# Kernel optimization log

Hardware: AMD Instinct MI355X
Metric: run time of the kernel (lower is better)

## Reference

```python
import jax, jax.numpy as jnp
import numpy as np

DIM = 3072
HEADS = 24
HD = 128
FF = 4 * DIM
EPS = 1e-6
SCALE_SHIFT = 1.0


def _ln(x):
    # LayerNorm, elementwise_affine=False
    mu = jnp.mean(x, axis=-1, keepdims=True)
    var = jnp.mean(jnp.square(x - mu), axis=-1, keepdims=True)
    return (x - mu) * jax.lax.rsqrt(var + EPS)


def _rms(x, w):
    # RMSNorm over head_dim with learned weight
    ms = jnp.mean(jnp.square(x), axis=-1, keepdims=True)
    return x * jax.lax.rsqrt(ms + EPS) * w


def _rope(x, cos, sin):
    # x: [B,S,H,D], cos/sin: [S,D]; interleaved rotate-half (diffusers style)
    xr = x.reshape(*x.shape[:-1], -1, 2)
    x1, x2 = xr[..., 0], xr[..., 1]
    rot = jnp.stack([-x2, x1], axis=-1).reshape(x.shape)
    return x * cos[None, :, None, :] + rot * sin[None, :, None, :]


def _mod_params(temb, w, b):
    m = jax.nn.silu(temb) @ w + b  # [B, 6*DIM]
    B = m.shape[0]
    m = m.reshape(B, -1, 6).transpose(0, 2, 1).reshape(B, -1)  # reorder to 6 blocks of DIM
    return jnp.split(m, 2, axis=-1)  # mod1, mod2 each [B, 3*DIM]


def _modulate(x, mp):
    shift, scale, gate = jnp.split(mp, 3, axis=-1)
    scale = scale + SCALE_SHIFT
    return x * scale[:, None, :] + shift[:, None, :], gate[:, None, :]


def setup_inputs() -> dict:
    key = jax.random.key(0)
    ks = jax.random.split(key, 32)
    B, ST, SI = 1, 512, 1024
    S = ST + SI
    r = lambda k, shp, s=1.0: jax.random.normal(k, shp, dtype=jnp.float32) * s
    W = 0.02  # weight init scale
    ang = jax.random.uniform(ks[5], (S, HD), minval=0.0, maxval=2 * np.pi)
    inp = {
        "hidden_states": r(ks[0], (B, SI, DIM)),
        "encoder_hidden_states": r(ks[1], (B, ST, DIM)),
        "encoder_hidden_states_mask": jnp.ones((B, ST), jnp.float32),
        "temb": r(ks[2], (B, DIM)),
        "rope_cos": jnp.cos(ang),
        "rope_sin": jnp.sin(ang),
        "w_img_mod": r(ks[6], (DIM, 6 * DIM), W), "b_img_mod": r(ks[7], (6 * DIM,), W),
        "w_txt_mod": r(ks[8], (DIM, 6 * DIM), W), "b_txt_mod": r(ks[9], (6 * DIM,), W),
        "norm_q_w": jnp.ones((HD,), jnp.float32), "norm_k_w": jnp.ones((HD,), jnp.float32),
        "norm_added_q_w": jnp.ones((HD,), jnp.float32), "norm_added_k_w": jnp.ones((HD,), jnp.float32),
        "w_qkv": r(ks[10], (DIM, 3 * DIM), W), "b_qkv": r(ks[11], (3 * DIM,), W),
        "w_add_qkv": r(ks[12], (DIM, 3 * DIM), W), "b_add_qkv": r(ks[13], (3 * DIM,), W),
        "w_out": r(ks[14], (DIM, DIM), W), "b_out": r(ks[15], (DIM,), W),
        "w_add_out": r(ks[16], (DIM, DIM), W), "b_add_out": r(ks[17], (DIM,), W),
        "w_img_mlp1": r(ks[18], (DIM, FF), W), "b_img_mlp1": r(ks[19], (FF,), W),
        "w_img_mlp2": r(ks[20], (FF, DIM), W), "b_img_mlp2": r(ks[21], (DIM,), W),
        "w_txt_mlp1": r(ks[22], (DIM, FF), W), "b_txt_mlp1": r(ks[23], (FF,), W),
        "w_txt_mlp2": r(ks[24], (FF, DIM), W), "b_txt_mlp2": r(ks[25], (DIM,), W),
    }
    return inp


def reference(hidden_states, encoder_hidden_states, encoder_hidden_states_mask, temb,
              rope_cos, rope_sin,
              w_img_mod, b_img_mod, w_txt_mod, b_txt_mod,
              norm_q_w, norm_k_w, norm_added_q_w, norm_added_k_w,
              w_qkv, b_qkv, w_add_qkv, b_add_qkv,
              w_out, b_out, w_add_out, b_add_out,
              w_img_mlp1, b_img_mlp1, w_img_mlp2, b_img_mlp2,
              w_txt_mlp1, b_txt_mlp1, w_txt_mlp2, b_txt_mlp2):
    B, SI, _ = hidden_states.shape
    ST = encoder_hidden_states.shape[1]

    img_mod1, img_mod2 = _mod_params(temb, w_img_mod, b_img_mod)
    txt_mod1, txt_mod2 = _mod_params(temb, w_txt_mod, b_txt_mod)

    img_m, img_g1 = _modulate(_ln(hidden_states), img_mod1)
    txt_m, txt_g1 = _modulate(_ln(encoder_hidden_states), txt_mod1)

    # joint attention
    iq, ik, iv = jnp.split(img_m @ w_qkv + b_qkv, 3, axis=-1)
    tq, tk, tv = jnp.split(txt_m @ w_add_qkv + b_add_qkv, 3, axis=-1)
    iq = _rms(iq.reshape(B, SI, HEADS, HD), norm_q_w)
    ik = _rms(ik.reshape(B, SI, HEADS, HD), norm_k_w)
    iv = iv.reshape(B, SI, HEADS, HD)
    tq = _rms(tq.reshape(B, ST, HEADS, HD), norm_added_q_w)
    tk = _rms(tk.reshape(B, ST, HEADS, HD), norm_added_k_w)
    tv = tv.reshape(B, ST, HEADS, HD)
    q = jnp.concatenate([tq, iq], axis=1)  # [B,S,H,D], txt first
    k = jnp.concatenate([tk, ik], axis=1)
    v = jnp.concatenate([tv, iv], axis=1)
    q = _rope(q, rope_cos, rope_sin)
    k = _rope(k, rope_cos, rope_sin)
    scores = jnp.einsum('bqhd,bkhd->bhqk', q, k) / np.float32(np.sqrt(HD))
    probs = jax.nn.softmax(scores, axis=-1)
    attn = jnp.einsum('bhqk,bkhd->bqhd', probs, v).reshape(B, ST + SI, HEADS * HD)

    txt_a = attn[:, :ST] @ w_add_out + b_add_out
    img_a = attn[:, ST:] @ w_out + b_out
    hidden = hidden_states + img_g1 * img_a
    enc = encoder_hidden_states + txt_g1 * txt_a

    # fused GELU(tanh) MLPs with modulation
    img_m2, img_g2 = _modulate(_ln(hidden), img_mod2)
    img_mlp = jax.nn.gelu(img_m2 @ w_img_mlp1 + b_img_mlp1, approximate=True) @ w_img_mlp2 + b_img_mlp2
    hidden = hidden + img_g2 * img_mlp

    txt_m2, txt_g2 = _modulate(_ln(enc), txt_mod2)
    txt_mlp = jax.nn.gelu(txt_m2 @ w_txt_mlp1 + b_txt_mlp1, approximate=True) @ w_txt_mlp2 + b_txt_mlp2
    enc = enc + txt_g2 * txt_mlp

    return enc, hidden
```

## Files before the change

### kernel.cpp

```cpp
#include <hip/hip_runtime.h>

#define DIMX 3072
#define STX 512
#define SIX 1024
#define SQX 1536
#define FFX 12288

typedef __attribute__((ext_vector_type(4))) float f32x4;
typedef __attribute__((ext_vector_type(8))) __bf16 bf16x8;
typedef __attribute__((ext_vector_type(4))) int i32x4;
typedef __attribute__((ext_vector_type(4))) unsigned short u16x4;

__device__ __forceinline__ unsigned short f2bf(float f){
  unsigned u = __builtin_bit_cast(unsigned, f);
  u += 0x7FFFu + ((u>>16)&1u);
  return (unsigned short)(u>>16);
}
__device__ __forceinline__ unsigned short usbf(float x){
  return __builtin_bit_cast(unsigned short, (__bf16)x);
}
__device__ __forceinline__ float bf2f(unsigned short h){
  unsigned u = ((unsigned)h)<<16;
  return __builtin_bit_cast(float, u);
}
__device__ __forceinline__ float gelu_tanh(float x){
  float x3 = x*x*x;
  float z = 0.7978845608028654f*(x + 0.044715f*x3);
  z = fminf(fmaxf(z, -15.f), 15.f);
  float e = exp2f(z*2.8853900817779268f);
  float th = (e-1.f)/(e+1.f);
  return 0.5f*x*(1.f+th);
}

__device__ __forceinline__ void gload16(const void* g, void* l){
  __builtin_amdgcn_global_load_lds(
      (const __attribute__((address_space(1))) void*)g,
      (__attribute__((address_space(3))) void*)l,
      16, 0, 0);
}


__global__ void k_silu(const float* __restrict__ temb, float* __restrict__ out){
  int i = blockIdx.x*256 + threadIdx.x;
  if(i < DIMX){
    float x = temb[i];
    out[i] = x / (1.f + exp2f(-x*1.4426950408889634f));
  }
}

__global__ void k_modinit(const float* __restrict__ b_img, const float* __restrict__ b_txt,
                          float* __restrict__ mod){
  int idx = blockIdx.x*256 + threadIdx.x;
  int mat = idx / 18432; int r = idx % 18432;
  int i = r/6, j = r%6;
  const float* b = mat ? b_txt : b_img;
  mod[mat*18432 + j*3072 + i] = b[r];
}

__global__ void k_modgemv(const float* __restrict__ w_img, const float* __restrict__ w_txt,
                          const float* __restrict__ silu_t, float* __restrict__ mod){
  int bz = blockIdx.x;
  int ks = bz & 7; bz >>= 3;
  int nc = bz % 18; int mat = bz / 18;
  const float* W = mat ? w_txt : w_img;
  __shared__ float st[384];
  int k0 = ks*384;
  for(int i = threadIdx.x; i < 384; i += 256) st[i] = silu_t[k0+i];
  __syncthreads();
  int n0 = nc*1024 + threadIdx.x*4;
  float ax=0.f, ay=0.f, az=0.f, aw=0.f;
  const float* Wp = W + (size_t)k0*18432 + n0;
  #pragma unroll 4
  for(int k=0;k<384;k++){
    float4 w = *(const float4*)(Wp + (size_t)k*18432);
    float s = st[k];
    ax += s*w.x; ay += s*w.y; az += s*w.z; aw += s*w.w;
  }
  float* md = mod + mat*18432;
  float vals[4] = {ax, ay, az, aw};
  #pragma unroll
  for(int j=0;j<4;j++){
    int n = n0+j; int i = n/6, jj = n%6;
    atomicAdd(&md[jj*3072 + i], vals[j]);
  }
}

__global__ void k_initC(float* __restrict__ out, const float* __restrict__ res,
                        const float* __restrict__ gate, const float* __restrict__ bias){
  int i = (blockIdx.x*256 + threadIdx.x)*4;
  int col = i % 3072;
  float4 r = *(const float4*)(res + i);
  float4 g = *(const float4*)(gate + col);
  float4 b = *(const float4*)(bias + col);
  float4 o = {r.x + g.x*b.x, r.y + g.y*b.y, r.z + g.z*b.z, r.w + g.w*b.w};
  *(float4*)(out + i) = o;
}

__global__ void k_lnmod(const float* __restrict__ x, const float* __restrict__ modp,
                        unsigned short* __restrict__ out){
  int row = blockIdx.x, t = threadIdx.x;
  const float* xr = x + (size_t)row*DIMX;
  float4 v0 = *(const float4*)(xr + t*4);
  float4 v1 = *(const float4*)(xr + 1024 + t*4);
  float4 v2 = *(const float4*)(xr + 2048 + t*4);
  float s  = v0.x+v0.y+v0.z+v0.w + v1.x+v1.y+v1.z+v1.w + v2.x+v2.y+v2.z+v2.w;
  float s2 = v0.x*v0.x+v0.y*v0.y+v0.z*v0.z+v0.w*v0.w
           + v1.x*v1.x+v1.y*v1.y+v1.z*v1.z+v1.w*v1.w
           + v2.x*v2.x+v2.y*v2.y+v2.z*v2.z+v2.w*v2.w;
  #pragma unroll
  for(int o=32;o>0;o>>=1){ s += __shfl_xor(s,o); s2 += __shfl_xor(s2,o); }
  __shared__ float rs_[4], rs2_[4];
  int wid = t>>6;
  if((t&63)==0){ rs_[wid]=s; rs2_[wid]=s2; }
  __syncthreads();
  float S  = rs_[0]+rs_[1]+rs_[2]+rs_[3];
  float S2 = rs2_[0]+rs2_[1]+rs2_[2]+rs2_[3];
  float mu = S*(1.f/3072.f);
  float var = S2*(1.f/3072.f) - mu*mu;
  float rstd = rsqrtf(var + 1e-6f);
  #pragma unroll
  for(int j=0;j<3;j++){
    int c = j*1024 + t*4;
    float4 sh = *(const float4*)(modp + c);
    float4 sc = *(const float4*)(modp + 3072 + c);
    float4 xv = (j==0)?v0:((j==1)?v1:v2);
    unsigned short h0 = f2bf((xv.x-mu)*rstd*(sc.x+1.f)+sh.x);
    unsigned short h1 = f2bf((xv.y-mu)*rstd*(sc.y+1.f)+sh.y);
    unsigned short h2 = f2bf((xv.z-mu)*rstd*(sc.z+1.f)+sh.z);
    unsigned short h3 = f2bf((xv.w-mu)*rstd*(sc.w+1.f)+sh.w);
    unsigned long long pk = (unsigned long long)(h0 | ((unsigned)h1<<16))
                          | ((unsigned long long)(h2 | ((unsigned)h3<<16))<<32);
    *(unsigned long long*)(out + (size_t)row*DIMX + c) = pk;
  }
}

__global__ void k_rmsrope(const unsigned short* __restrict__ qkv_txt,
                          const unsigned short* __restrict__ qkv_img,
                          const float* __restrict__ nqw, const float* __restrict__ nkw,
                          const float* __restrict__ naqw, const float* __restrict__ nakw,
                          const float* __restrict__ cosb, const float* __restrict__ sinb,
                          unsigned short* __restrict__ Q, unsigned short* __restrict__ K,
                          unsigned short* __restrict__ V){
  int s = blockIdx.x, h = blockIdx.y, t = threadIdx.x;
  bool txt = s < STX;
  const unsigned short* src = txt ? (qkv_txt + (size_t)s*9216)
                                  : (qkv_img + (size_t)(s-STX)*9216);
  const float* qw = txt ? naqw : nqw;
  const float* kw = txt ? nakw : nkw;
  int d0 = 2*t;
  float q1 = bf2f(src[h*128 + d0]),        q2 = bf2f(src[h*128 + d0 + 1]);
  float k1 = bf2f(src[3072 + h*128 + d0]), k2 = bf2f(src[3072 + h*128 + d0 + 1]);
  float v1 = bf2f(src[6144 + h*128 + d0]), v2 = bf2f(src[6144 + h*128 + d0 + 1]);
  float sq = q1*q1 + q2*q2, sk = k1*k1 + k2*k2;
  #pragma unroll
  for(int o=32;o>0;o>>=1){ sq += __shfl_xor(sq,o); sk += __shfl_xor(sk,o); }
  float rq = rsqrtf(sq*(1.f/128.f) + 1e-6f);
  float rk = rsqrtf(sk*(1.f/128.f) + 1e-6f);
  q1 *= rq*qw[d0]; q2 *= rq*qw[d0+1];
  k1 *= rk*kw[d0]; k2 *= rk*kw[d0+1];
  float c1 = cosb[(size_t)s*128 + d0], c2 = cosb[(size_t)s*128 + d0 + 1];
  float s1 = sinb[(size_t)s*128 + d0], s2 = sinb[(size_t)s*128 + d0 + 1];
  float Q1 = q1*c1 - q2*s1, Q2 = q2*c2 + q1*s2;
  float K1 = k1*c1 - k2*s1, K2 = k2*c2 + k1*s2;
  size_t o = ((size_t)s*24 + h)*128 + d0;
  Q[o] = f2bf(Q1); Q[o+1] = f2bf(Q2);
  K[o] = f2bf(K1); K[o+1] = f2bf(K2);
  V[o] = f2bf(v1); V[o+1] = f2bf(v2);
}

__global__ void k_vtrans(const unsigned short* __restrict__ V, unsigned short* __restrict__ VT){
  __shared__ unsigned short tile[64][136];
  int st = blockIdx.x, h = blockIdx.y, t = threadIdx.x;
  int s0 = st*64;
  {
    int s = t>>2;
    #pragma unroll
    for(int i=0;i<4;i++){
      int oct = ((t&3)<<2) + i;
      i32x4 d = *(const i32x4*)(V + ((size_t)(s0+s)*24 + h)*128 + oct*8);
      *(i32x4*)&tile[s][oct*8] = d;
    }
  }
  __syncthreads();
  {
    int d0 = t>>3; int strip = t&7;
    #pragma unroll
    for(int i=0;i<4;i++){
      int d = d0 + i*32;
      unsigned short h8[8];
      #pragma unroll
      for(int j=0;j<8;j++) h8[j] = tile[strip*8 + j][d];
      unsigned a0 = h8[0] | ((unsigned)h8[1]<<16);
      unsigned a1 = h8[2] | ((unsigned)h8[3]<<16);
      unsigned a2 = h8[4] | ((unsigned)h8[5]<<16);
      unsigned a3 = h8[6] | ((unsigned)h8[7]<<16);
      i32x4 dv = {(int)a0,(int)a1,(int)a2,(int)a3};
      *(i32x4*)(VT + ((size_t)h*128 + d)*1536 + s0 + strip*8) = dv;
    }
  }
}

__global__ __launch_bounds__(256,2) void k_fattn(
    const unsigned short* __restrict__ Q,
    const unsigned short* __restrict__ Kb,
    const unsigned short* __restrict__ VT,
    unsigned short* __restrict__ O)
{
  __shared__ unsigned short Kls[4][64][32];
  __shared__ unsigned short Vls[2][128][32];
  __shared__ unsigned short Pls[128][72];
  const int t = threadIdx.x;
  const int qb = blockIdx.x, h = blockIdx.y;
  const int lane = t&63, w = t>>6;
  const int lr = lane&15, lk = lane>>4;
  const float SC  = 0.08838834764831845f;
  const float L2E = 1.4426950408889634f;

  bf16x8 qf[2][4];
  {
    const unsigned short* qp = Q + ((size_t)(qb*128 + w*32 + lr)*3072) + h*128 + lk*8;
    #pragma unroll
    for(int mf=0;mf<2;mf++)
      #pragma unroll
      for(int ks=0;ks<4;ks++)
        qf[mf][ks] = *(const bf16x8*)(qp + (size_t)mf*16*3072 + ks*32);
  }

  f32x4 o[2][8];
  #pragma unroll
  for(int i=0;i<2;i++)
    #pragma unroll
    for(int j=0;j<8;j++) o[i][j] = (f32x4){0.f,0.f,0.f,0.f};
  float mrow[2][4], lrow[2][4];
  #pragma unroll
  for(int i=0;i<2;i++)
    #pragma unroll
    for(int r=0;r<4;r++){ mrow[i][r] = -3.0e30f; lrow[i][r] = 0.f; }

  for(int kv0=0; kv0<SQX; kv0+=64){
    __syncthreads();
    {
      const unsigned short* kp = Kb + ((size_t)(kv0 + (lane>>2))*3072) + h*128 + w*32 + (lane&3)*8;
      #pragma unroll
      for(int i=0;i<4;i++)
        gload16(kp + (size_t)i*16*3072, &Kls[w][i*16][0]);
    }
    {
      int c = w>>1;
      const unsigned short* vp = VT + ((size_t)(h*128 + (w&1)*64 + (lane>>2)))*1536 + kv0 + c*32 + (lane&3)*8;
      #pragma unroll
      for(int j=0;j<4;j++)
        gload16(vp + (size_t)j*16*1536, &Vls[c][(w&1)*64 + j*16][0]);
    }
    __syncthreads();

    f32x4 s[2][4];
    #pragma unroll
    for(int mf=0;mf<2;mf++)
      #pragma unroll
      for(int nf=0;nf<4;nf++) s[mf][nf] = (f32x4){0.f,0.f,0.f,0.f};
    #pragma unroll
    for(int ks=0;ks<4;ks++){
      bf16x8 kf[4];
      #pragma unroll
      for(int nf=0;nf<4;nf++) kf[nf] = *(const bf16x8*)&Kls[ks][nf*16+lr][lk*8];
      #pragma unroll
      for(int mf=0;mf<2;mf++)
        #pragma unroll
        for(int nf=0;nf<4;nf++)
          s[mf][nf] = __builtin_amdgcn_mfma_f32_16x16x32_bf16(qf[mf][ks], kf[nf], s[mf][nf], 0,0,0);
    }

    #pragma unroll
    for(int mf=0;mf<2;mf++){
      #pragma unroll
      for(int r=0;r<4;r++){
        float v = fmaxf(fmaxf(s[mf][0][r], s[mf][1][r]), fmaxf(s[mf][2][r], s[mf][3][r]));
        #pragma unroll
        for(int d=1; d<16; d<<=1) v = fmaxf(v, __shfl_xor(v, d));
        float nm = fmaxf(mrow[mf][r], v*SC);
        float fac = exp2f((mrow[mf][r]-nm)*L2E);
        mrow[mf][r] = nm;
        float rs = 0.f;
        #pragma unroll
        for(int nf=0;nf<4;nf++){
          float p = exp2f((s[mf][nf][r]*SC - nm)*L2E);
          s[mf][nf][r] = p;
          rs += p;
        }
        #pragma unroll
        for(int d=1; d<16; d<<=1) rs += __shfl_xor(rs, d);
        lrow[mf][r] = lrow[mf][r]*fac + rs;
        #pragma unroll
        for(int nf=0;nf<8;nf++) o[mf][nf][r] *= fac;
      }
    }

    #pragma unroll
    for(int mf=0;mf<2;mf++)
      #pragma unroll
      for(int nf=0;nf<4;nf++)
        #pragma unroll
        for(int r=0;r<4;r++)
          Pls[w*32 + mf*16 + lk*4 + r][nf*16 + lr] = usbf(s[mf][nf][r]);

    #pragma unroll
    for(int ks2=0; ks2<2; ks2++){
      bf16x8 pa[2];
      #pragma unroll
      for(int mf=0;mf<2;mf++)
        pa[mf] = *(const bf16x8*)&Pls[w*32 + mf*16 + lr][ks2*32 + lk*8];
      #pragma unroll
      for(int nf=0;nf<8;nf++){
        bf16x8 vf = *(const bf16x8*)&Vls[ks2][nf*16+lr][lk*8];
        #pragma unroll
        for(int mf=0;mf<2;mf++)
          o[mf][nf] = __builtin_amdgcn_mfma_f32_16x16x32_bf16(pa[mf], vf, o[mf][nf], 0,0,0);
      }
    }
  }

  #pragma unroll
  for(int mf=0;mf<2;mf++){
    float inv[4];
    #pragma unroll
    for(int r=0;r<4;r++) inv[r] = 1.f/lrow[mf][r];
    #pragma unroll
    for(int nf=0;nf<8;nf++){
      #pragma unroll
      for(int r=0;r<4;r++){
        size_t row = (size_t)qb*128 + w*32 + mf*16 + lk*4 + r;
        size_t col = (size_t)h*128 + nf*16 + lr;
        O[row*3072 + col] = usbf(o[mf][nf][r]*inv[r]);
      }
    }
  }
}

__global__ __launch_bounds__(256,4) void k_gemmW(
    const unsigned short* __restrict__ A, long lda,
    const float* __restrict__ W, long ldw,
    const float* __restrict__ bias,
    void* __restrict__ Cp, long ldc,
    int K, int KS, int mode,
    const float* __restrict__ gate)
{
  __shared__ unsigned short Als[128*32];
  __shared__ float Wls[32*128];
  __shared__ unsigned short Bls[128*40];
  const int t = threadIdx.x;
  const int bn = blockIdx.x, bm = blockIdx.y;
  const int zs = blockIdx.z;
  const int Kc = K / KS, kbeg = zs*Kc, kend = kbeg + Kc;

  const unsigned short* Ab = A + (size_t)bm*128*lda;
  const float* Wb = W + (size_t)bn*128;

  const int lane = t & 63, wid = t>>6, wr = wid>>1, wc = wid&1;
  const int lr = lane & 15, lk = lane>>4;
  const int srow = (lane>>2);
  const int soff = (lane&3)*8;
  const int wrow = (lane>>5);
  const int wcol = (lane&31)*4;
  const int ck = (t&7)*4;
  const int cn = (t>>3)*4;

  f32x4 acc[4][4];
  #pragma unroll
  for(int i=0;i<4;i++)
    #pragma unroll
    for(int j=0;j<4;j++) acc[i][j] = {0.f,0.f,0.f,0.f};

  for(int k0=kbeg; k0<kend; k0+=32){
    __syncthreads();
    gload16(Ab + (size_t)(     wid*16 + srow)*lda + k0 + soff, Als + (     wid*16)*32);
    gload16(Ab + (size_t)(64 + wid*16 + srow)*lda + k0 + soff, Als + (64 + wid*16)*32);
    #pragma unroll
    for(int i=0;i<4;i++){
      int r0 = wid*8 + i*2;
      gload16(Wb + (size_t)(k0 + r0 + wrow)*ldw + wcol, Wls + r0*128);
    }
    __syncthreads();
    {
      f32x4 r0 = *(const f32x4*)&Wls[(ck+0)*128 + cn];
      f32x4 r1 = *(const f32x4*)&Wls[(ck+1)*128 + cn];
      f32x4 r2 = *(const f32x4*)&Wls[(ck+2)*128 + cn];
      f32x4 r3 = *(const f32x4*)&Wls[(ck+3)*128 + cn];
      #pragma unroll
      for(int jn=0;jn<4;jn++){
        u16x4 pk = { usbf(r0[jn]), usbf(r1[jn]), usbf(r2[jn]), usbf(r3[jn]) };
        *(u16x4*)&Bls[(cn+jn)*40 + ck] = pk;
      }
    }
    __syncthreads();
    bf16x8 af[4], bfr[4];
    #pragma unroll
    for(int mf=0;mf<4;mf++) af[mf]  = *(const bf16x8*)&Als[(wr*64 + mf*16 + lr)*32 + lk*8];
    #pragma unroll
    for(int nf=0;nf<4;nf++) bfr[nf] = *(const bf16x8*)&Bls[(wc*64 + nf*16 + lr)*40 + lk*8];
    #pragma unroll
    for(int mf=0;mf<4;mf++)
      #pragma unroll
      for(int nf=0;nf<4;nf++)
        acc[mf][nf] = __builtin_amdgcn_mfma_f32_16x16x32_bf16(af[mf], bfr[nf], acc[mf][nf], 0,0,0);
  }

  unsigned short* C16 = (unsigned short*)Cp;
  float* C32 = (float*)Cp;
  #pragma unroll
  for(int mf=0;mf<4;mf++){
    #pragma unroll
    for(int nf=0;nf<4;nf++){
      #pragma unroll
      for(int r=0;r<4;r++){
        size_t row = (size_t)bm*128 + wr*64 + mf*16 + lk*4 + r;
        size_t col = (size_t)bn*128 + wc*64 + nf*16 + lr;
        float v = acc[mf][nf][r];
        if(mode==0){
          C16[row*ldc + col] = f2bf(v + (bias ? bias[col] : 0.f));
        } else if(mode==1){
          C16[row*ldc + col] = f2bf(gelu_tanh(v + (bias ? bias[col] : 0.f)));
        } else {
          float g = gate ? gate[col] : 1.f;
          atomicAdd(&C32[row*ldc + col], g*v);
        }
      }
    }
  }
}


extern "C" void kernel_launch(void* const* d_in, const int* in_sizes, int n_in,
                              void* d_out, int out_size, void* d_ws, size_t ws_size,
                              hipStream_t stream){
  const float* hidden_states = (const float*)d_in[0];
  const float* enc_states    = (const float*)d_in[1];
  const float* temb          = (const float*)d_in[3];
  const float* rope_cos      = (const float*)d_in[4];
  const float* rope_sin      = (const float*)d_in[5];
  const float* w_img_mod     = (const float*)d_in[6];
  const float* b_img_mod     = (const float*)d_in[7];
  const float* w_txt_mod     = (const float*)d_in[8];
  const float* b_txt_mod     = (const float*)d_in[9];
  const float* norm_q_w      = (const float*)d_in[10];
  const float* norm_k_w      = (const float*)d_in[11];
  const float* norm_aq_w     = (const float*)d_in[12];
  const float* norm_ak_w     = (const float*)d_in[13];
  const float* w_qkv   = (const float*)d_in[14];
  const float* b_qkv   = (const float*)d_in[15];
  const float* w_aqkv  = (const float*)d_in[16];
  const float* b_aqkv  = (const float*)d_in[17];
  const float* w_out_  = (const float*)d_in[18];
  const float* b_out_  = (const float*)d_in[19];
  const float* w_aout  = (const float*)d_in[20];
  const float* b_aout  = (const float*)d_in[21];
  const float* w_mlp1i = (const float*)d_in[22];
  const float* b_mlp1i = (const float*)d_in[23];
  const float* w_mlp2i = (const float*)d_in[24];
  const float* b_mlp2i = (const float*)d_in[25];
  const float* w_mlp1t = (const float*)d_in[26];
  const float* b_mlp1t = (const float*)d_in[27];
  const float* w_mlp2t = (const float*)d_in[28];
  const float* b_mlp2t = (const float*)d_in[29];

  char* ws = (char*)d_ws;
  float* mod    = (float*)(ws + 0);
  float* silu_t = (float*)(ws + 147456);
  unsigned short* imgm = (unsigned short*)(ws + 159744);
  unsigned short* txtm = (unsigned short*)(ws + 6451200);
  float* hid = (float*)(ws + 9596928);
  float* enc = (float*)(ws + 22179840);
  unsigned short* Qb  = (unsigned short*)(ws + 47345664);
  unsigned short* Kb  = (unsigned short*)(ws + 56782848);
  unsigned short* Vb  = (unsigned short*)(ws + 66220032);
  unsigned short* attnb = (unsigned short*)(ws + 66220032);
  unsigned short* VTb = (unsigned short*)(ws + 75657216);
  unsigned short* qkvi = (unsigned short*)(ws + 141717504);
  unsigned short* qkvt = (unsigned short*)(ws + 160591872);
  unsigned short* mlph = (unsigned short*)(ws + 103968768);

  float* out_enc = (float*)d_out;
  float* out_hid = (float*)d_out + (size_t)STX*DIMX;

  k_silu<<<12,256,0,stream>>>(temb, silu_t);
  k_modinit<<<144,256,0,stream>>>(b_img_mod, b_txt_mod, mod);
  k_modgemv<<<288,256,0,stream>>>(w_img_mod, w_txt_mod, silu_t, mod);

  k_lnmod<<<SIX,256,0,stream>>>(hidden_states, mod + 0,     imgm);
  k_lnmod<<<STX,256,0,stream>>>(enc_states,    mod + 18432, txtm);

  k_gemmW<<<dim3(72,8,1),256,0,stream>>>(imgm,3072, w_qkv,9216, b_qkv,
      qkvi,9216, 3072,1, 0, nullptr);
  k_gemmW<<<dim3(72,4,1),256,0,stream>>>(txtm,3072, w_aqkv,9216, b_aqkv,
      qkvt,9216, 3072,1, 0, nullptr);

  k_rmsrope<<<dim3(1536,24),64,0,stream>>>(qkvt, qkvi, norm_q_w, norm_k_w,
      norm_aq_w, norm_ak_w, rope_cos, rope_sin, Qb, Kb, Vb);
  k_vtrans<<<dim3(24,24),256,0,stream>>>(Vb, VTb);

  k_fattn<<<dim3(12,24),256,0,stream>>>(Qb, Kb, VTb, attnb);

  k_initC<<<512*3,256,0,stream>>>(enc, enc_states, mod + 18432 + 2*3072, b_aout);
  k_initC<<<1024*3,256,0,stream>>>(hid, hidden_states, mod + 2*3072, b_out_);
  k_gemmW<<<dim3(24,4,8),256,0,stream>>>(attnb,3072, w_aout,3072, nullptr,
      enc,3072, 3072,8, 3, mod + 18432 + 2*3072);
  k_gemmW<<<dim3(24,8,4),256,0,stream>>>(attnb + (size_t)512*3072,3072, w_out_,3072, nullptr,
      hid,3072, 3072,4, 3, mod + 2*3072);

  k_lnmod<<<SIX,256,0,stream>>>(hid, mod + 3*3072, imgm);
  k_gemmW<<<dim3(96,8,1),256,0,stream>>>(imgm,3072, w_mlp1i,12288, b_mlp1i,
      mlph,12288, 3072,1, 1, nullptr);
  k_initC<<<1024*3,256,0,stream>>>(out_hid, hid, mod + 5*3072, b_mlp2i);
  k_gemmW<<<dim3(24,8,4),256,0,stream>>>(mlph,12288, w_mlp2i,3072, nullptr,
      out_hid,3072, 12288,4, 3, mod + 5*3072);

  k_lnmod<<<STX,256,0,stream>>>(enc, mod + 18432 + 3*3072, txtm);
  k_gemmW<<<dim3(96,4,1),256,0,stream>>>(txtm,3072, w_mlp1t,12288, b_mlp1t,
      mlph,12288, 3072,1, 1, nullptr);
  k_initC<<<512*3,256,0,stream>>>(out_enc, enc, mod + 18432 + 5*3072, b_mlp2t);
  k_gemmW<<<dim3(24,4,8),256,0,stream>>>(mlph,12288, w_mlp2t,3072, nullptr,
      out_enc,3072, 12288,8, 3, mod + 18432 + 5*3072);
}
```

Before: 1.251 ms.

## Double-buffer k_gemmW shared tiles and convert fp32 weights in registers

Rewrites the k_gemmW main loop to double-buffer the A and bf16 B tiles in LDS. The next K-slice is prefetched while MFMAs run on the current one, and the loop drops from three barriers per step to one. Weights are now loaded straight into registers as float4, converted to bf16 and stored transposed into LDS, so the fp32 weight staging buffer goes away. The cost is more register pressure from the prefetched weights and a second set of LDS buffers, which could lower occupancy under launch_bounds(256,4).

After: 1.195 ms. 1.05x faster.

```diff
diff --git a/kernel.cpp b/kernel.cpp
--- a/kernel.cpp
+++ b/kernel.cpp
@@ -345,9 +345,8 @@
     int K, int KS, int mode,
     const float* __restrict__ gate)
 {
-  __shared__ unsigned short Als[128*32];
-  __shared__ float Wls[32*128];
-  __shared__ unsigned short Bls[128*40];
+  __shared__ unsigned short Als[2][128*32];
+  __shared__ unsigned short Bls[2][128*40];
   const int t = threadIdx.x;
   const int bn = blockIdx.x, bm = blockIdx.y;
   const int zs = blockIdx.z;
@@ -360,10 +359,8 @@
   const int lr = lane & 15, lk = lane>>4;
   const int srow = (lane>>2);
   const int soff = (lane&3)*8;
-  const int wrow = (lane>>5);
-  const int wcol = (lane&31)*4;
-  const int ck = (t&7)*4;
-  const int cn = (t>>3)*4;
+  const int wcb = (t&31)*4;
+  const int wrb = (t>>5)*4;
 
   f32x4 acc[4][4];
   #pragma unroll
@@ -371,38 +368,56 @@
     #pragma unroll
     for(int j=0;j<4;j++) acc[i][j] = {0.f,0.f,0.f,0.f};
 
+  float4 wreg[4];
+
+  gload16(Ab + (size_t)(     wid*16 + srow)*lda + kbeg + soff, &Als[0][(     wid*16)*32]);
+  gload16(Ab + (size_t)(64 + wid*16 + srow)*lda + kbeg + soff, &Als[0][(64 + wid*16)*32]);
+  #pragma unroll
+  for(int j=0;j<4;j++)
+    wreg[j] = *(const float4*)(Wb + (size_t)(kbeg + wrb + j)*ldw + wcb);
+  #pragma unroll
+  for(int i=0;i<4;i++){
+    u16x4 pk = { usbf(wreg[0][i]), usbf(wreg[1][i]), usbf(wreg[2][i]), usbf(wreg[3][i]) };
+    *(u16x4*)&Bls[0][(wcb+i)*40 + wrb] = pk;
+  }
+  __syncthreads();
+
+  unsigned short* AlsC = &Als[0][0]; unsigned short* AlsN = &Als[1][0];
+  unsigned short* BlsC = &Bls[0][0]; unsigned short* BlsN = &Bls[1][0];
+
   for(int k0=kbeg; k0<kend; k0+=32){
+    const bool has = (k0 + 32 < kend);
+    if(has){
+      int kn = k0 + 32;
+      gload16(Ab + (size_t)(     wid*16 + srow)*lda + kn + soff, AlsN + (     wid*16)*32);
+      gload16(Ab + (size_t)(64 + wid*16 + srow)*lda + kn + soff, AlsN + (64 + wid*16)*32);
+      #pragma unroll
+      for(int j=0;j<4;j++)
+        wreg[j] = *(const float4*)(Wb + (size_t)(kn + wrb + j)*ldw + wcb);
+    }
+    {
+      bf16x8 af[4], bfr[4];
+      #pragma unroll
+      for(int mf=0;mf<4;mf++) af[mf]  = *(const bf16x8*)&AlsC[(wr*64 + mf*16 + lr)*32 + lk*8];
+      #pragma unroll
+      for(int nf=0;nf<4;nf++) bfr[nf] = *(const bf16x8*)&BlsC[(wc*64 + nf*16 + lr)*40 + lk*8];
+      #pragma unroll
+      for(int mf=0;mf<4;mf++)
+        #pragma unroll
+        for(int nf=0;nf<4;nf++)
+          acc[mf][nf] = __builtin_amdgcn_mfma_f32_16x16x32_bf16(af[mf], bfr[nf], acc[mf][nf], 0,0,0);
+    }
+    if(has){
+      #pragma unroll
+      for(int i=0;i<4;i++){
+        u16x4 pk = { usbf(wreg[0][i]), usbf(wreg[1][i]), usbf(wreg[2][i]), usbf(wreg[3][i]) };
+        *(u16x4*)&BlsN[(wcb+i)*40 + wrb] = pk;
+      }
+    }
     __syncthreads();
-    gload16(Ab + (size_t)(     wid*16 + srow)*lda + k0 + soff, Als + (     wid*16)*32);
-    gload16(Ab + (size_t)(64 + wid*16 + srow)*lda + k0 + soff, Als + (64 + wid*16)*32);
-    #pragma unroll
-    for(int i=0;i<4;i++){
-      int r0 = wid*8 + i*2;
-      gload16(Wb + (size_t)(k0 + r0 + wrow)*ldw + wcol, Wls + r0*128);
-    }
-    __syncthreads();
-    {
-      f32x4 r0 = *(const f32x4*)&Wls[(ck+0)*128 + cn];
-      f32x4 r1 = *(const f32x4*)&Wls[(ck+1)*128 + cn];
-      f32x4 r2 = *(const f32x4*)&Wls[(ck+2)*128 + cn];
-      f32x4 r3 = *(const f32x4*)&Wls[(ck+3)*128 + cn];
-      #pragma unroll
-      for(int jn=0;jn<4;jn++){
-        u16x4 pk = { usbf(r0[jn]), usbf(r1[jn]), usbf(r2[jn]), usbf(r3[jn]) };
-        *(u16x4*)&Bls[(cn+jn)*40 + ck] = pk;
-      }
-    }
-    __syncthreads();
-    bf16x8 af[4], bfr[4];
-    #pragma unroll
-    for(int mf=0;mf<4;mf++) af[mf]  = *(const bf16x8*)&Als[(wr*64 + mf*16 + lr)*32 + lk*8];
-    #pragma unroll
-    for(int nf=0;nf<4;nf++) bfr[nf] = *(const bf16x8*)&Bls[(wc*64 + nf*16 + lr)*40 + lk*8];
-    #pragma unroll
-    for(int mf=0;mf<4;mf++)
-      #pragma unroll
-      for(int nf=0;nf<4;nf++)
-        acc[mf][nf] = __builtin_amdgcn_mfma_f32_16x16x32_bf16(af[mf], bfr[nf], acc[mf][nf], 0,0,0);
+    unsigned short* tmp;
+    tmp = AlsC; AlsC = AlsN; AlsN = tmp;
+    tmp = BlsC; BlsC = BlsN; BlsN = tmp;
   }
 
   unsigned short* C16 = (unsigned short*)Cp;
```
